# Kernel tuning notes

Hardware: AMD Instinct MI355X
Metric: run time of the kernel (lower is better)

Reference implementation:

```python
import jax, jax.numpy as jnp
import numpy as np

B, A, D, H = 2048, 32, 128, 256

def setup_inputs() -> dict:
    key = jax.random.key(0)
    ks = jax.random.split(key, 12)
    s = lambda fan_in: 1.0 / np.sqrt(fan_in)
    return {
        "obs": jax.random.normal(ks[0], (B, A, D), dtype=jnp.float32),
        "act": jax.random.normal(ks[1], (B, A, 8), dtype=jnp.float32),
        "enc_W": jax.random.uniform(ks[2], (H, D), jnp.float32, -s(D), s(D)),
        "enc_b": jax.random.uniform(ks[3], (H,), jnp.float32, -s(D), s(D)),
        "fobs_W": jax.random.uniform(ks[4], (H, H), jnp.float32, -s(H), s(H)),
        "fobs_b": jax.random.uniform(ks[5], (H,), jnp.float32, -s(H), s(H)),
        "W_ih": jax.random.uniform(ks[6], (3 * H, H), jnp.float32, -s(H), s(H)),
        "b_ih": jax.random.uniform(ks[7], (3 * H,), jnp.float32, -s(H), s(H)),
        "W_hh": jax.random.uniform(ks[8], (3 * H, H), jnp.float32, -s(H), s(H)),
        "b_hh": jax.random.uniform(ks[9], (3 * H,), jnp.float32, -s(H), s(H)),
        "dec_W": jax.random.uniform(ks[10], (1, H), jnp.float32, -s(H), s(H)),
        "dec_b": jax.random.uniform(ks[11], (1,), jnp.float32, -s(H), s(H)),
    }

def _gru_cell(x, h, W_ih, b_ih, W_hh, b_hh):
    # torch.nn.GRUCell: gates stacked as [reset, update, new]
    gi = x @ W_ih.T + b_ih          # [N, 3H]
    gh = h @ W_hh.T + b_hh          # [N, 3H]
    i_r, i_z, i_n = jnp.split(gi, 3, axis=-1)
    h_r, h_z, h_n = jnp.split(gh, 3, axis=-1)
    r = jax.nn.sigmoid(i_r + h_r)
    z = jax.nn.sigmoid(i_z + h_z)
    n = jnp.tanh(i_n + r * h_n)
    return (1.0 - z) * n + z * h

def reference(obs, act, enc_W, enc_b, fobs_W, fobs_b, W_ih, b_ih, W_hh, b_hh, dec_W, dec_b):
    b, a, d = obs.shape
    x = obs.reshape(b * a, d)                         # [B*A, D]
    e = jax.nn.relu(x @ enc_W.T + enc_b)              # encoder + ReLU
    h = e @ fobs_W.T + fobs_b                         # h_out
    # k = 0: comm input is zeros
    h = _gru_cell(jnp.zeros_like(h), h, W_ih, b_ih, W_hh, b_hh)
    # k = 1: masked mean over other agents == (sum_j h_j - h_i) / n_agents
    hA = h.reshape(b, a, -1)                          # [B, A, H]
    c = (hA.sum(axis=1, keepdims=True) - hA) / a      # [B, A, H]
    h = _gru_cell(c.reshape(b * a, -1), h, W_ih, b_ih, W_hh, b_hh)
    return (h @ dec_W.T + dec_b).reshape(b, a, -1)    # [B, A, 1]
```

## Files before the change

kernel.cpp:

```cpp
#include <hip/hip_runtime.h>
#include <hip/hip_fp16.h>


#define NB   2048
#define NA   32
#define DIN  128
#define HID  256
#define SA   264
#define MROWS 64

typedef _Float16 half8  __attribute__((ext_vector_type(8)));
typedef float    float4v __attribute__((ext_vector_type(4)));

#define ENC_OFF    0
#define FOBS_OFF   32768
#define WIH_OFF    98304
#define WHH_OFF    294912
#define PREP_TOTAL 491520

__global__ void prep_weights(const float* __restrict__ encW, const float* __restrict__ fobsW,
                             const float* __restrict__ wih,  const float* __restrict__ whh,
                             _Float16* __restrict__ prep) {
    int G = blockIdx.x * 256 + threadIdx.x;
    if (G >= PREP_TOTAL / 8) return;
    int F = G << 3;
    const float* src; int K, local = F, nt, ks;
    if (F < FOBS_OFF) {
        src = encW;  K = 128;
        int t = local >> 9; nt = t & 15; ks = t >> 4;
    } else if (F < WIH_OFF) {
        src = fobsW; K = 256; local = F - FOBS_OFF;
        int t = local >> 9; nt = t & 15; ks = t >> 4;
    } else if (F < WHH_OFF) {
        src = wih;   K = 256; local = F - WIH_OFF;
        int t = local >> 9; nt = t % 48; ks = t / 48;
    } else {
        src = whh;   K = 256; local = F - WHH_OFF;
        int t = local >> 9; nt = t % 48; ks = t / 48;
    }
    int lane = (local >> 3) & 63;
    int col  = nt * 16 + (lane & 15);
    int k    = ks * 32 + ((lane >> 4) << 3);
    const float* s = src + col * K + k;
    float4v v0 = *(const float4v*)(s);
    float4v v1 = *(const float4v*)(s + 4);
    half8 hv;
    hv[0] = (_Float16)v0[0]; hv[1] = (_Float16)v0[1];
    hv[2] = (_Float16)v0[2]; hv[3] = (_Float16)v0[3];
    hv[4] = (_Float16)v1[0]; hv[5] = (_Float16)v1[1];
    hv[6] = (_Float16)v1[2]; hv[7] = (_Float16)v1[3];
    *(half8*)(prep + F) = hv;
}

__device__ __forceinline__ float sigmoid_f(float x) {
    return 1.f / (1.f + __expf(-x));
}
__device__ __forceinline__ float tanh_f(float x) {
    return 1.f - 2.f / (__expf(2.f * x) + 1.f);
}

__device__ __forceinline__ half8 ldB(const _Float16* __restrict__ prepm, int NT, int nt, int ks,
                                     const float* __restrict__ raw, int K, int use_prep, int lane) {
    if (use_prep)
        return *(const half8*)(prepm + (((ks * NT + nt) * 64 + lane) << 3));
    half8 b;
    int l16 = lane & 15, kq = (lane >> 4) << 3;
    #pragma unroll
    for (int j = 0; j < 8; j++)
        b[j] = (_Float16)raw[(nt * 16 + l16) * K + ks * 32 + kq + j];
    return b;
}

__global__ __launch_bounds__(1024) void commnet_fused(
    const float* __restrict__ obs, const _Float16* __restrict__ prep,
    const float* __restrict__ enc_b, const float* __restrict__ fobs_b,
    const float* __restrict__ b_ih, const float* __restrict__ b_hh,
    const float* __restrict__ dec_W, const float* __restrict__ dec_b,
    float* __restrict__ out,
    const float* __restrict__ encW, const float* __restrict__ fobsW,
    const float* __restrict__ wih, const float* __restrict__ whh,
    int use_prep)
{
    const int b    = blockIdx.x;
    const int tid  = threadIdx.x;
    const int lane = tid & 63;
    const int nt   = tid >> 6;
    const int l16  = lane & 15;
    const int quad = lane >> 4;
    const int kq   = quad << 3;
    const int col  = nt * 16 + l16;

    __shared__ __align__(16) _Float16 sA[3][MROWS * SA];
    __shared__ float Srow[MROWS];

    {
        const float* obsb = obs + (size_t)b * MROWS * DIN;
        int r   = tid >> 4;
        int off = (tid & 15) << 3;
        const float* src = obsb + r * DIN + off;
        float4v v0 = *(const float4v*)(src);
        float4v v1 = *(const float4v*)(src + 4);
        half8 hv;
        hv[0] = (_Float16)v0[0]; hv[1] = (_Float16)v0[1];
        hv[2] = (_Float16)v0[2]; hv[3] = (_Float16)v0[3];
        hv[4] = (_Float16)v1[0]; hv[5] = (_Float16)v1[1];
        hv[6] = (_Float16)v1[2]; hv[7] = (_Float16)v1[3];
        *(half8*)(&sA[0][r * SA + off]) = hv;
        if (tid < MROWS) Srow[tid] = 0.f;
    }
    __syncthreads();

    {
        float4v acc[4];
        float4v z = {0.f, 0.f, 0.f, 0.f};
        acc[0] = z; acc[1] = z; acc[2] = z; acc[3] = z;
        #pragma unroll
        for (int ks = 0; ks < 4; ks++) {
            int kbase = ks * 32 + kq;
            half8 Af[4];
            #pragma unroll
            for (int mt = 0; mt < 4; mt++)
                Af[mt] = *(const half8*)(&sA[0][(mt * 16 + l16) * SA + kbase]);
            half8 b0 = ldB(prep + ENC_OFF, 16, nt, ks, encW, DIN, use_prep, lane);
            #pragma unroll
            for (int mt = 0; mt < 4; mt++)
                acc[mt] = __builtin_amdgcn_mfma_f32_16x16x32_f16(Af[mt], b0, acc[mt], 0, 0, 0);
        }
        float bb = enc_b[col];
        #pragma unroll
        for (int mt = 0; mt < 4; mt++)
            #pragma unroll
            for (int r = 0; r < 4; r++) {
                int row = mt * 16 + quad * 4 + r;
                sA[1][row * SA + col] = (_Float16)fmaxf(acc[mt][r] + bb, 0.f);
            }
    }
    __syncthreads();

    float4v hacc[4];
    {
        float4v z = {0.f, 0.f, 0.f, 0.f};
        hacc[0] = z; hacc[1] = z; hacc[2] = z; hacc[3] = z;
        #pragma unroll 2
        for (int ks = 0; ks < 8; ks++) {
            int kbase = ks * 32 + kq;
            half8 Af[4];
            #pragma unroll
            for (int mt = 0; mt < 4; mt++)
                Af[mt] = *(const half8*)(&sA[1][(mt * 16 + l16) * SA + kbase]);
            half8 b0 = ldB(prep + FOBS_OFF, 16, nt, ks, fobsW, HID, use_prep, lane);
            #pragma unroll
            for (int mt = 0; mt < 4; mt++)
                hacc[mt] = __builtin_amdgcn_mfma_f32_16x16x32_f16(Af[mt], b0, hacc[mt], 0, 0, 0);
        }
        float bb = fobs_b[col];
        #pragma unroll
        for (int mt = 0; mt < 4; mt++)
            #pragma unroll
            for (int r = 0; r < 4; r++) {
                int row = mt * 16 + quad * 4 + r;
                float h = hacc[mt][r] + bb;
                hacc[mt][r] = h;
                sA[0][row * SA + col] = (_Float16)h;
            }
    }
    __syncthreads();

    #pragma unroll 1
    for (int half = 0; half < 2; half++) {
        const int rb = half * 32;
        float4v aR[2], aZ[2], aN[2];
        float4v z = {0.f, 0.f, 0.f, 0.f};
        aR[0] = z; aR[1] = z; aZ[0] = z; aZ[1] = z; aN[0] = z; aN[1] = z;
        #pragma unroll 2
        for (int ks = 0; ks < 8; ks++) {
            const int kbase = ks * 32 + kq;
            half8 A0 = *(const half8*)(&sA[0][(rb + l16) * SA + kbase]);
            half8 A1 = *(const half8*)(&sA[0][(rb + 16 + l16) * SA + kbase]);
            half8 bR = ldB(prep + WHH_OFF, 48,  0 + nt, ks, whh, HID, use_prep, lane);
            half8 bZ = ldB(prep + WHH_OFF, 48, 16 + nt, ks, whh, HID, use_prep, lane);
            half8 bN = ldB(prep + WHH_OFF, 48, 32 + nt, ks, whh, HID, use_prep, lane);
            aR[0] = __builtin_amdgcn_mfma_f32_16x16x32_f16(A0, bR, aR[0], 0, 0, 0);
            aR[1] = __builtin_amdgcn_mfma_f32_16x16x32_f16(A1, bR, aR[1], 0, 0, 0);
            aZ[0] = __builtin_amdgcn_mfma_f32_16x16x32_f16(A0, bZ, aZ[0], 0, 0, 0);
            aZ[1] = __builtin_amdgcn_mfma_f32_16x16x32_f16(A1, bZ, aZ[1], 0, 0, 0);
            aN[0] = __builtin_amdgcn_mfma_f32_16x16x32_f16(A0, bN, aN[0], 0, 0, 0);
            aN[1] = __builtin_amdgcn_mfma_f32_16x16x32_f16(A1, bN, aN[1], 0, 0, 0);
        }
        float biR = b_ih[col],       bhR = b_hh[col];
        float biZ = b_ih[256 + col], bhZ = b_hh[256 + col];
        float biN = b_ih[512 + col], bhN = b_hh[512 + col];
        float h1v[2][4];
        float psum = 0.f;
        #pragma unroll
        for (int mt = 0; mt < 2; mt++)
            #pragma unroll
            for (int r = 0; r < 4; r++) {
                int row = rb + mt * 16 + quad * 4 + r;
                float rg = sigmoid_f(biR + aR[mt][r] + bhR);
                float zg = sigmoid_f(biZ + aZ[mt][r] + bhZ);
                float ng = tanh_f(biN + rg * (aN[mt][r] + bhN));
                float hold = hacc[half * 2 + mt][r];
                float h1 = (1.f - zg) * ng + zg * hold;
                h1v[mt][r] = h1;
                sA[1][row * SA + col] = (_Float16)h1;
                psum += h1;
            }
        psum += __shfl_xor(psum, 16);
        psum += __shfl_xor(psum, 32);
        #pragma unroll
        for (int mt = 0; mt < 2; mt++)
            #pragma unroll
            for (int r = 0; r < 4; r++) {
                int row = rb + mt * 16 + quad * 4 + r;
                sA[2][row * SA + col] = (_Float16)((psum - h1v[mt][r]) * (1.f / 32.f));
            }
    }
    __syncthreads();

    #pragma unroll 1
    for (int half = 0; half < 2; half++) {
        const int rb = half * 32;
        float4v aR[2], aZ[2], aNi[2], aNh[2];
        float4v z = {0.f, 0.f, 0.f, 0.f};
        aR[0] = z; aR[1] = z; aZ[0] = z; aZ[1] = z;
        aNi[0] = z; aNi[1] = z; aNh[0] = z; aNh[1] = z;
        #pragma unroll 1
        for (int ks = 0; ks < 8; ks++) {
            const int kbase = ks * 32 + kq;
            {
                half8 C0 = *(const half8*)(&sA[2][(rb + l16) * SA + kbase]);
                half8 C1 = *(const half8*)(&sA[2][(rb + 16 + l16) * SA + kbase]);
                half8 bR = ldB(prep + WIH_OFF, 48,  0 + nt, ks, wih, HID, use_prep, lane);
                half8 bZ = ldB(prep + WIH_OFF, 48, 16 + nt, ks, wih, HID, use_prep, lane);
                half8 bN = ldB(prep + WIH_OFF, 48, 32 + nt, ks, wih, HID, use_prep, lane);
                aR[0]  = __builtin_amdgcn_mfma_f32_16x16x32_f16(C0, bR, aR[0], 0, 0, 0);
                aR[1]  = __builtin_amdgcn_mfma_f32_16x16x32_f16(C1, bR, aR[1], 0, 0, 0);
                aZ[0]  = __builtin_amdgcn_mfma_f32_16x16x32_f16(C0, bZ, aZ[0], 0, 0, 0);
                aZ[1]  = __builtin_amdgcn_mfma_f32_16x16x32_f16(C1, bZ, aZ[1], 0, 0, 0);
                aNi[0] = __builtin_amdgcn_mfma_f32_16x16x32_f16(C0, bN, aNi[0], 0, 0, 0);
                aNi[1] = __builtin_amdgcn_mfma_f32_16x16x32_f16(C1, bN, aNi[1], 0, 0, 0);
            }
            {
                half8 H0 = *(const half8*)(&sA[1][(rb + l16) * SA + kbase]);
                half8 H1 = *(const half8*)(&sA[1][(rb + 16 + l16) * SA + kbase]);
                half8 bR = ldB(prep + WHH_OFF, 48,  0 + nt, ks, whh, HID, use_prep, lane);
                half8 bZ = ldB(prep + WHH_OFF, 48, 16 + nt, ks, whh, HID, use_prep, lane);
                half8 bN = ldB(prep + WHH_OFF, 48, 32 + nt, ks, whh, HID, use_prep, lane);
                aR[0]  = __builtin_amdgcn_mfma_f32_16x16x32_f16(H0, bR, aR[0], 0, 0, 0);
                aR[1]  = __builtin_amdgcn_mfma_f32_16x16x32_f16(H1, bR, aR[1], 0, 0, 0);
                aZ[0]  = __builtin_amdgcn_mfma_f32_16x16x32_f16(H0, bZ, aZ[0], 0, 0, 0);
                aZ[1]  = __builtin_amdgcn_mfma_f32_16x16x32_f16(H1, bZ, aZ[1], 0, 0, 0);
                aNh[0] = __builtin_amdgcn_mfma_f32_16x16x32_f16(H0, bN, aNh[0], 0, 0, 0);
                aNh[1] = __builtin_amdgcn_mfma_f32_16x16x32_f16(H1, bN, aNh[1], 0, 0, 0);
            }
        }

        float biR = b_ih[col],       bhR = b_hh[col];
        float biZ = b_ih[256 + col], bhZ = b_hh[256 + col];
        float biN = b_ih[512 + col], bhN = b_hh[512 + col];
        float dw  = dec_W[col];
        float p[2][4];
        #pragma unroll
        for (int mt = 0; mt < 2; mt++)
            #pragma unroll
            for (int r = 0; r < 4; r++) {
                int row = rb + mt * 16 + quad * 4 + r;
                float rg = sigmoid_f(aR[mt][r] + biR + bhR);
                float zg = sigmoid_f(aZ[mt][r] + biZ + bhZ);
                float ng = tanh_f((aNi[mt][r] + biN) + rg * (aNh[mt][r] + bhN));
                float h1v = (float)sA[1][row * SA + col];
                float h2 = (1.f - zg) * ng + zg * h1v;
                p[mt][r] = h2 * dw;
            }
        #pragma unroll
        for (int m = 1; m <= 8; m <<= 1) {
            #pragma unroll
            for (int mt = 0; mt < 2; mt++)
                #pragma unroll
                for (int r = 0; r < 4; r++)
                    p[mt][r] += __shfl_xor(p[mt][r], m);
        }
        if (l16 == 0) {
            #pragma unroll
            for (int mt = 0; mt < 2; mt++)
                #pragma unroll
                for (int r = 0; r < 4; r++)
                    atomicAdd(&Srow[rb + mt * 16 + quad * 4 + r], p[mt][r]);
        }
    }
    __syncthreads();
    if (tid < MROWS) out[(size_t)b * MROWS + tid] = Srow[tid] + dec_b[0];
}

extern "C" void kernel_launch(void* const* d_in, const int* in_sizes, int n_in,
                              void* d_out, int out_size, void* d_ws, size_t ws_size,
                              hipStream_t stream) {
    const float* obs   = (const float*)d_in[0];
    const float* encW  = (const float*)d_in[2];
    const float* encb  = (const float*)d_in[3];
    const float* fobsW = (const float*)d_in[4];
    const float* fobsb = (const float*)d_in[5];
    const float* wih   = (const float*)d_in[6];
    const float* bih   = (const float*)d_in[7];
    const float* whh   = (const float*)d_in[8];
    const float* bhh   = (const float*)d_in[9];
    const float* decW  = (const float*)d_in[10];
    const float* decb  = (const float*)d_in[11];
    float* out = (float*)d_out;

    _Float16* prep = (_Float16*)d_ws;
    int use_prep = (ws_size >= (size_t)PREP_TOTAL * sizeof(_Float16)) ? 1 : 0;
    if (use_prep) {
        prep_weights<<<(PREP_TOTAL / 8 + 255) / 256, 256, 0, stream>>>(encW, fobsW, wih, whh, prep);
    }
    commnet_fused<<<NB / 2, 1024, 0, stream>>>(obs, prep, encb, fobsb, bih, bhh, decW, decb, out,
                                               encW, fobsW, wih, whh, use_prep);
}
```

Baseline: 238.2 us.

## Process four batches per block to amortize weight loads across more rows

Each block now handles 128 rows (four batch elements) instead of 64, halving the grid so every weight fragment loaded from global memory feeds twice as many MFMAs. To fit in LDS, the third shared buffer is dropped: the comm input is rebuilt in place from per-group column sums stored in a small float array, and the old hidden state is re-read as fp16 from shared memory rather than kept in fp32 registers. In exchange, fewer blocks cover the device, the reused hidden state loses precision, and extra barriers and passes are added.

```diff
diff --git a/kernel.cpp b/kernel.cpp
--- a/kernel.cpp
+++ b/kernel.cpp
@@ -7,7 +7,7 @@
 #define DIN  128
 #define HID  256
 #define SA   264
-#define MROWS 64
+#define MROWS 128
 
 typedef _Float16 half8  __attribute__((ext_vector_type(8)));
 typedef float    float4v __attribute__((ext_vector_type(4)));
@@ -90,27 +90,34 @@
     const int kq   = quad << 3;
     const int col  = nt * 16 + l16;
 
-    __shared__ __align__(16) _Float16 sA[3][MROWS * SA];
+    __shared__ __align__(16) _Float16 sA[2][MROWS * SA];
+    __shared__ __align__(16) float Scol[4][HID];
     __shared__ float Srow[MROWS];
 
     {
         const float* obsb = obs + (size_t)b * MROWS * DIN;
-        int r   = tid >> 4;
-        int off = (tid & 15) << 3;
-        const float* src = obsb + r * DIN + off;
-        float4v v0 = *(const float4v*)(src);
-        float4v v1 = *(const float4v*)(src + 4);
-        half8 hv;
-        hv[0] = (_Float16)v0[0]; hv[1] = (_Float16)v0[1];
-        hv[2] = (_Float16)v0[2]; hv[3] = (_Float16)v0[3];
-        hv[4] = (_Float16)v1[0]; hv[5] = (_Float16)v1[1];
-        hv[6] = (_Float16)v1[2]; hv[7] = (_Float16)v1[3];
-        *(half8*)(&sA[0][r * SA + off]) = hv;
+        #pragma unroll
+        for (int it = 0; it < 2; it++) {
+            int i   = tid + it * 1024;
+            int r   = i >> 4;
+            int off = (i & 15) << 3;
+            const float* src = obsb + r * DIN + off;
+            float4v v0 = *(const float4v*)(src);
+            float4v v1 = *(const float4v*)(src + 4);
+            half8 hv;
+            hv[0] = (_Float16)v0[0]; hv[1] = (_Float16)v0[1];
+            hv[2] = (_Float16)v0[2]; hv[3] = (_Float16)v0[3];
+            hv[4] = (_Float16)v1[0]; hv[5] = (_Float16)v1[1];
+            hv[6] = (_Float16)v1[2]; hv[7] = (_Float16)v1[3];
+            *(half8*)(&sA[0][r * SA + off]) = hv;
+        }
         if (tid < MROWS) Srow[tid] = 0.f;
     }
     __syncthreads();
 
-    {
+    #pragma unroll 1
+    for (int hp = 0; hp < 2; hp++) {
+        const int rb = hp * 64;
         float4v acc[4];
         float4v z = {0.f, 0.f, 0.f, 0.f};
         acc[0] = z; acc[1] = z; acc[2] = z; acc[3] = z;
@@ -120,7 +127,7 @@
             half8 Af[4];
             #pragma unroll
             for (int mt = 0; mt < 4; mt++)
-                Af[mt] = *(const half8*)(&sA[0][(mt * 16 + l16) * SA + kbase]);
+                Af[mt] = *(const half8*)(&sA[0][(rb + mt * 16 + l16) * SA + kbase]);
             half8 b0 = ldB(prep + ENC_OFF, 16, nt, ks, encW, DIN, use_prep, lane);
             #pragma unroll
             for (int mt = 0; mt < 4; mt++)
@@ -131,44 +138,44 @@
         for (int mt = 0; mt < 4; mt++)
             #pragma unroll
             for (int r = 0; r < 4; r++) {
-                int row = mt * 16 + quad * 4 + r;
+                int row = rb + mt * 16 + quad * 4 + r;
                 sA[1][row * SA + col] = (_Float16)fmaxf(acc[mt][r] + bb, 0.f);
             }
     }
     __syncthreads();
 
-    float4v hacc[4];
-    {
+    #pragma unroll 1
+    for (int hp = 0; hp < 2; hp++) {
+        const int rb = hp * 64;
+        float4v acc[4];
         float4v z = {0.f, 0.f, 0.f, 0.f};
-        hacc[0] = z; hacc[1] = z; hacc[2] = z; hacc[3] = z;
+        acc[0] = z; acc[1] = z; acc[2] = z; acc[3] = z;
         #pragma unroll 2
         for (int ks = 0; ks < 8; ks++) {
             int kbase = ks * 32 + kq;
             half8 Af[4];
             #pragma unroll
             for (int mt = 0; mt < 4; mt++)
-                Af[mt] = *(const half8*)(&sA[1][(mt * 16 + l16) * SA + kbase]);
+                Af[mt] = *(const half8*)(&sA[1][(rb + mt * 16 + l16) * SA + kbase]);
             half8 b0 = ldB(prep + FOBS_OFF, 16, nt, ks, fobsW, HID, use_prep, lane);
             #pragma unroll
             for (int mt = 0; mt < 4; mt++)
-                hacc[mt] = __builtin_amdgcn_mfma_f32_16x16x32_f16(Af[mt], b0, hacc[mt], 0, 0, 0);
+                acc[mt] = __builtin_amdgcn_mfma_f32_16x16x32_f16(Af[mt], b0, acc[mt], 0, 0, 0);
         }
         float bb = fobs_b[col];
         #pragma unroll
         for (int mt = 0; mt < 4; mt++)
             #pragma unroll
             for (int r = 0; r < 4; r++) {
-                int row = mt * 16 + quad * 4 + r;
-                float h = hacc[mt][r] + bb;
-                hacc[mt][r] = h;
-                sA[0][row * SA + col] = (_Float16)h;
+                int row = rb + mt * 16 + quad * 4 + r;
+                sA[0][row * SA + col] = (_Float16)(acc[mt][r] + bb);
             }
     }
     __syncthreads();
 
     #pragma unroll 1
-    for (int half = 0; half < 2; half++) {
-        const int rb = half * 32;
+    for (int q = 0; q < 4; q++) {
+        const int rb = q * 32;
         float4v aR[2], aZ[2], aN[2];
         float4v z = {0.f, 0.f, 0.f, 0.f};
         aR[0] = z; aR[1] = z; aZ[0] = z; aZ[1] = z; aN[0] = z; aN[1] = z;
@@ -190,7 +197,6 @@
         float biR = b_ih[col],       bhR = b_hh[col];
         float biZ = b_ih[256 + col], bhZ = b_hh[256 + col];
         float biN = b_ih[512 + col], bhN = b_hh[512 + col];
-        float h1v[2][4];
         float psum = 0.f;
         #pragma unroll
         for (int mt = 0; mt < 2; mt++)
@@ -200,27 +206,44 @@
                 float rg = sigmoid_f(biR + aR[mt][r] + bhR);
                 float zg = sigmoid_f(biZ + aZ[mt][r] + bhZ);
                 float ng = tanh_f(biN + rg * (aN[mt][r] + bhN));
-                float hold = hacc[half * 2 + mt][r];
+                float hold = (float)sA[0][row * SA + col];
                 float h1 = (1.f - zg) * ng + zg * hold;
-                h1v[mt][r] = h1;
                 sA[1][row * SA + col] = (_Float16)h1;
                 psum += h1;
             }
         psum += __shfl_xor(psum, 16);
         psum += __shfl_xor(psum, 32);
-        #pragma unroll
-        for (int mt = 0; mt < 2; mt++)
-            #pragma unroll
-            for (int r = 0; r < 4; r++) {
-                int row = rb + mt * 16 + quad * 4 + r;
-                sA[2][row * SA + col] = (_Float16)((psum - h1v[mt][r]) * (1.f / 32.f));
-            }
+        if (lane < 16) Scol[q][nt * 16 + lane] = psum;
+    }
+    __syncthreads();
+
+    {
+        #pragma unroll
+        for (int it = 0; it < 4; it++) {
+            int i  = tid + it * 1024;
+            int r  = i >> 5;
+            int c8 = (i & 31) << 3;
+            const float* Sp = &Scol[r >> 5][0];
+            half8 hv = *(const half8*)(&sA[1][r * SA + c8]);
+            float4v t0 = *(const float4v*)(Sp + c8);
+            float4v t1 = *(const float4v*)(Sp + c8 + 4);
+            half8 cv;
+            cv[0] = (_Float16)((t0[0] - (float)hv[0]) * (1.f / 32.f));
+            cv[1] = (_Float16)((t0[1] - (float)hv[1]) * (1.f / 32.f));
+            cv[2] = (_Float16)((t0[2] - (float)hv[2]) * (1.f / 32.f));
+            cv[3] = (_Float16)((t0[3] - (float)hv[3]) * (1.f / 32.f));
+            cv[4] = (_Float16)((t1[0] - (float)hv[4]) * (1.f / 32.f));
+            cv[5] = (_Float16)((t1[1] - (float)hv[5]) * (1.f / 32.f));
+            cv[6] = (_Float16)((t1[2] - (float)hv[6]) * (1.f / 32.f));
+            cv[7] = (_Float16)((t1[3] - (float)hv[7]) * (1.f / 32.f));
+            *(half8*)(&sA[0][r * SA + c8]) = cv;
+        }
     }
     __syncthreads();
 
     #pragma unroll 1
-    for (int half = 0; half < 2; half++) {
-        const int rb = half * 32;
+    for (int q = 0; q < 4; q++) {
+        const int rb = q * 32;
         float4v aR[2], aZ[2], aNi[2], aNh[2];
         float4v z = {0.f, 0.f, 0.f, 0.f};
         aR[0] = z; aR[1] = z; aZ[0] = z; aZ[1] = z;
@@ -229,8 +252,8 @@
         for (int ks = 0; ks < 8; ks++) {
             const int kbase = ks * 32 + kq;
             {
-                half8 C0 = *(const half8*)(&sA[2][(rb + l16) * SA + kbase]);
-                half8 C1 = *(const half8*)(&sA[2][(rb + 16 + l16) * SA + kbase]);
+                half8 C0 = *(const half8*)(&sA[0][(rb + l16) * SA + kbase]);
+                half8 C1 = *(const half8*)(&sA[0][(rb + 16 + l16) * SA + kbase]);
                 half8 bR = ldB(prep + WIH_OFF, 48,  0 + nt, ks, wih, HID, use_prep, lane);
                 half8 bZ = ldB(prep + WIH_OFF, 48, 16 + nt, ks, wih, HID, use_prep, lane);
                 half8 bN = ldB(prep + WIH_OFF, 48, 32 + nt, ks, wih, HID, use_prep, lane);
@@ -314,6 +337,6 @@
     if (use_prep) {
         prep_weights<<<(PREP_TOTAL / 8 + 255) / 256, 256, 0, stream>>>(encW, fobsW, wih, whh, prep);
     }
-    commnet_fused<<<NB / 2, 1024, 0, stream>>>(obs, prep, encb, fobsb, bih, bhh, decW, decb, out,
+    commnet_fused<<<NB / 4, 1024, 0, stream>>>(obs, prep, encb, fobsb, bih, bhh, decW, decb, out,
                                                encW, fobsW, wih, whh, use_prep);
 }
```

Result: slower. 246.2 us (+3.4%).

## Retile fused kernel to one batch per 512-thread block with 2x2 MFMA tiles

Applied to the files above, without the earlier changes.

Each block now handles 32 rows (one batch element) with 8 waves instead of 64 rows with 16 waves, and every wave computes a 2x2 tile of 16x16 MFMA outputs covering two column tiles. This halves LDS per block, so more blocks can be resident per CU and the loop over two row halves disappears, giving more overlap across barriers. Each A fragment is now reused across two weight fragments in registers. The trade-off is that the full weight set is streamed once per 32 rows rather than once per 64 rows, which doubles total weight traffic from L2.

```diff
diff --git a/kernel.cpp b/kernel.cpp
--- a/kernel.cpp
+++ b/kernel.cpp
@@ -7,7 +7,7 @@
 #define DIN  128
 #define HID  256
 #define SA   264
-#define MROWS 64
+#define MROWS 32
 
 typedef _Float16 half8  __attribute__((ext_vector_type(8)));
 typedef float    float4v __attribute__((ext_vector_type(4)));
@@ -71,7 +71,7 @@
     return b;
 }
 
-__global__ __launch_bounds__(1024) void commnet_fused(
+__global__ __launch_bounds__(512) void commnet_fused(
     const float* __restrict__ obs, const _Float16* __restrict__ prep,
     const float* __restrict__ enc_b, const float* __restrict__ fobs_b,
     const float* __restrict__ b_ih, const float* __restrict__ b_hh,
@@ -84,11 +84,11 @@
     const int b    = blockIdx.x;
     const int tid  = threadIdx.x;
     const int lane = tid & 63;
-    const int nt   = tid >> 6;
+    const int w    = tid >> 6;
     const int l16  = lane & 15;
     const int quad = lane >> 4;
     const int kq   = quad << 3;
-    const int col  = nt * 16 + l16;
+    const int nt0  = w * 2;
 
     __shared__ __align__(16) _Float16 sA[3][MROWS * SA];
     __shared__ float Srow[MROWS];
@@ -111,168 +111,219 @@
     __syncthreads();
 
     {
-        float4v acc[4];
+        float4v acc[2][2];
         float4v z = {0.f, 0.f, 0.f, 0.f};
-        acc[0] = z; acc[1] = z; acc[2] = z; acc[3] = z;
+        acc[0][0] = z; acc[0][1] = z; acc[1][0] = z; acc[1][1] = z;
         #pragma unroll
         for (int ks = 0; ks < 4; ks++) {
             int kbase = ks * 32 + kq;
-            half8 Af[4];
-            #pragma unroll
-            for (int mt = 0; mt < 4; mt++)
-                Af[mt] = *(const half8*)(&sA[0][(mt * 16 + l16) * SA + kbase]);
-            half8 b0 = ldB(prep + ENC_OFF, 16, nt, ks, encW, DIN, use_prep, lane);
-            #pragma unroll
-            for (int mt = 0; mt < 4; mt++)
-                acc[mt] = __builtin_amdgcn_mfma_f32_16x16x32_f16(Af[mt], b0, acc[mt], 0, 0, 0);
-        }
-        float bb = enc_b[col];
-        #pragma unroll
-        for (int mt = 0; mt < 4; mt++)
-            #pragma unroll
-            for (int r = 0; r < 4; r++) {
-                int row = mt * 16 + quad * 4 + r;
-                sA[1][row * SA + col] = (_Float16)fmaxf(acc[mt][r] + bb, 0.f);
-            }
-    }
-    __syncthreads();
-
-    float4v hacc[4];
+            half8 A0 = *(const half8*)(&sA[0][(l16) * SA + kbase]);
+            half8 A1 = *(const half8*)(&sA[0][(16 + l16) * SA + kbase]);
+            half8 b0 = ldB(prep + ENC_OFF, 16, nt0,     ks, encW, DIN, use_prep, lane);
+            half8 b1 = ldB(prep + ENC_OFF, 16, nt0 + 1, ks, encW, DIN, use_prep, lane);
+            acc[0][0] = __builtin_amdgcn_mfma_f32_16x16x32_f16(A0, b0, acc[0][0], 0, 0, 0);
+            acc[0][1] = __builtin_amdgcn_mfma_f32_16x16x32_f16(A0, b1, acc[0][1], 0, 0, 0);
+            acc[1][0] = __builtin_amdgcn_mfma_f32_16x16x32_f16(A1, b0, acc[1][0], 0, 0, 0);
+            acc[1][1] = __builtin_amdgcn_mfma_f32_16x16x32_f16(A1, b1, acc[1][1], 0, 0, 0);
+        }
+        #pragma unroll
+        for (int nn = 0; nn < 2; nn++) {
+            int col = (nt0 + nn) * 16 + l16;
+            float bb = enc_b[col];
+            #pragma unroll
+            for (int mt = 0; mt < 2; mt++)
+                #pragma unroll
+                for (int r = 0; r < 4; r++) {
+                    int row = mt * 16 + quad * 4 + r;
+                    sA[1][row * SA + col] = (_Float16)fmaxf(acc[mt][nn][r] + bb, 0.f);
+                }
+        }
+    }
+    __syncthreads();
+
+    float4v hacc[2][2];
     {
         float4v z = {0.f, 0.f, 0.f, 0.f};
-        hacc[0] = z; hacc[1] = z; hacc[2] = z; hacc[3] = z;
+        hacc[0][0] = z; hacc[0][1] = z; hacc[1][0] = z; hacc[1][1] = z;
         #pragma unroll 2
         for (int ks = 0; ks < 8; ks++) {
             int kbase = ks * 32 + kq;
-            half8 Af[4];
-            #pragma unroll
-            for (int mt = 0; mt < 4; mt++)
-                Af[mt] = *(const half8*)(&sA[1][(mt * 16 + l16) * SA + kbase]);
-            half8 b0 = ldB(prep + FOBS_OFF, 16, nt, ks, fobsW, HID, use_prep, lane);
-            #pragma unroll
-            for (int mt = 0; mt < 4; mt++)
-                hacc[mt] = __builtin_amdgcn_mfma_f32_16x16x32_f16(Af[mt], b0, hacc[mt], 0, 0, 0);
-        }
-        float bb = fobs_b[col];
-        #pragma unroll
-        for (int mt = 0; mt < 4; mt++)
-            #pragma unroll
-            for (int r = 0; r < 4; r++) {
-                int row = mt * 16 + quad * 4 + r;
-                float h = hacc[mt][r] + bb;
-                hacc[mt][r] = h;
-                sA[0][row * SA + col] = (_Float16)h;
-            }
-    }
-    __syncthreads();
-
-    #pragma unroll 1
-    for (int half = 0; half < 2; half++) {
-        const int rb = half * 32;
-        float4v aR[2], aZ[2], aN[2];
+            half8 A0 = *(const half8*)(&sA[1][(l16) * SA + kbase]);
+            half8 A1 = *(const half8*)(&sA[1][(16 + l16) * SA + kbase]);
+            half8 b0 = ldB(prep + FOBS_OFF, 16, nt0,     ks, fobsW, HID, use_prep, lane);
+            half8 b1 = ldB(prep + FOBS_OFF, 16, nt0 + 1, ks, fobsW, HID, use_prep, lane);
+            hacc[0][0] = __builtin_amdgcn_mfma_f32_16x16x32_f16(A0, b0, hacc[0][0], 0, 0, 0);
+            hacc[0][1] = __builtin_amdgcn_mfma_f32_16x16x32_f16(A0, b1, hacc[0][1], 0, 0, 0);
+            hacc[1][0] = __builtin_amdgcn_mfma_f32_16x16x32_f16(A1, b0, hacc[1][0], 0, 0, 0);
+            hacc[1][1] = __builtin_amdgcn_mfma_f32_16x16x32_f16(A1, b1, hacc[1][1], 0, 0, 0);
+        }
+        #pragma unroll
+        for (int nn = 0; nn < 2; nn++) {
+            int col = (nt0 + nn) * 16 + l16;
+            float bb = fobs_b[col];
+            #pragma unroll
+            for (int mt = 0; mt < 2; mt++)
+                #pragma unroll
+                for (int r = 0; r < 4; r++) {
+                    int row = mt * 16 + quad * 4 + r;
+                    float h = hacc[mt][nn][r] + bb;
+                    hacc[mt][nn][r] = h;
+                    sA[0][row * SA + col] = (_Float16)h;
+                }
+        }
+    }
+    __syncthreads();
+
+    {
+        float4v aR[2][2], aZ[2][2], aN[2][2];
         float4v z = {0.f, 0.f, 0.f, 0.f};
-        aR[0] = z; aR[1] = z; aZ[0] = z; aZ[1] = z; aN[0] = z; aN[1] = z;
+        #pragma unroll
+        for (int mt = 0; mt < 2; mt++)
+            #pragma unroll
+            for (int nn = 0; nn < 2; nn++) { aR[mt][nn] = z; aZ[mt][nn] = z; aN[mt][nn] = z; }
         #pragma unroll 2
         for (int ks = 0; ks < 8; ks++) {
             const int kbase = ks * 32 + kq;
-            half8 A0 = *(const half8*)(&sA[0][(rb + l16) * SA + kbase]);
-            half8 A1 = *(const half8*)(&sA[0][(rb + 16 + l16) * SA + kbase]);
-            half8 bR = ldB(prep + WHH_OFF, 48,  0 + nt, ks, whh, HID, use_prep, lane);
-            half8 bZ = ldB(prep + WHH_OFF, 48, 16 + nt, ks, whh, HID, use_prep, lane);
-            half8 bN = ldB(prep + WHH_OFF, 48, 32 + nt, ks, whh, HID, use_prep, lane);
-            aR[0] = __builtin_amdgcn_mfma_f32_16x16x32_f16(A0, bR, aR[0], 0, 0, 0);
-            aR[1] = __builtin_amdgcn_mfma_f32_16x16x32_f16(A1, bR, aR[1], 0, 0, 0);
-            aZ[0] = __builtin_amdgcn_mfma_f32_16x16x32_f16(A0, bZ, aZ[0], 0, 0, 0);
-            aZ[1] = __builtin_amdgcn_mfma_f32_16x16x32_f16(A1, bZ, aZ[1], 0, 0, 0);
-            aN[0] = __builtin_amdgcn_mfma_f32_16x16x32_f16(A0, bN, aN[0], 0, 0, 0);
-            aN[1] = __builtin_amdgcn_mfma_f32_16x16x32_f16(A1, bN, aN[1], 0, 0, 0);
-        }
-        float biR = b_ih[col],       bhR = b_hh[col];
-        float biZ = b_ih[256 + col], bhZ = b_hh[256 + col];
-        float biN = b_ih[512 + col], bhN = b_hh[512 + col];
-        float h1v[2][4];
-        float psum = 0.f;
+            half8 A0 = *(const half8*)(&sA[0][(l16) * SA + kbase]);
+            half8 A1 = *(const half8*)(&sA[0][(16 + l16) * SA + kbase]);
+            half8 bR0 = ldB(prep + WHH_OFF, 48,  0 + nt0,     ks, whh, HID, use_prep, lane);
+            half8 bR1 = ldB(prep + WHH_OFF, 48,  0 + nt0 + 1, ks, whh, HID, use_prep, lane);
+            aR[0][0] = __builtin_amdgcn_mfma_f32_16x16x32_f16(A0, bR0, aR[0][0], 0, 0, 0);
+            aR[0][1] = __builtin_amdgcn_mfma_f32_16x16x32_f16(A0, bR1, aR[0][1], 0, 0, 0);
+            aR[1][0] = __builtin_amdgcn_mfma_f32_16x16x32_f16(A1, bR0, aR[1][0], 0, 0, 0);
+            aR[1][1] = __builtin_amdgcn_mfma_f32_16x16x32_f16(A1, bR1, aR[1][1], 0, 0, 0);
+            half8 bZ0 = ldB(prep + WHH_OFF, 48, 16 + nt0,     ks, whh, HID, use_prep, lane);
+            half8 bZ1 = ldB(prep + WHH_OFF, 48, 16 + nt0 + 1, ks, whh, HID, use_prep, lane);
+            aZ[0][0] = __builtin_amdgcn_mfma_f32_16x16x32_f16(A0, bZ0, aZ[0][0], 0, 0, 0);
+            aZ[0][1] = __builtin_amdgcn_mfma_f32_16x16x32_f16(A0, bZ1, aZ[0][1], 0, 0, 0);
+            aZ[1][0] = __builtin_amdgcn_mfma_f32_16x16x32_f16(A1, bZ0, aZ[1][0], 0, 0, 0);
+            aZ[1][1] = __builtin_amdgcn_mfma_f32_16x16x32_f16(A1, bZ1, aZ[1][1], 0, 0, 0);
+            half8 bN0 = ldB(prep + WHH_OFF, 48, 32 + nt0,     ks, whh, HID, use_prep, lane);
+            half8 bN1 = ldB(prep + WHH_OFF, 48, 32 + nt0 + 1, ks, whh, HID, use_prep, lane);
+            aN[0][0] = __builtin_amdgcn_mfma_f32_16x16x32_f16(A0, bN0, aN[0][0], 0, 0, 0);
+            aN[0][1] = __builtin_amdgcn_mfma_f32_16x16x32_f16(A0, bN1, aN[0][1], 0, 0, 0);
+            aN[1][0] = __builtin_amdgcn_mfma_f32_16x16x32_f16(A1, bN0, aN[1][0], 0, 0, 0);
+            aN[1][1] = __builtin_amdgcn_mfma_f32_16x16x32_f16(A1, bN1, aN[1][1], 0, 0, 0);
+        }
+        #pragma unroll
+        for (int nn = 0; nn < 2; nn++) {
+            int col = (nt0 + nn) * 16 + l16;
+            float biR = b_ih[col],       bhR = b_hh[col];
+            float biZ = b_ih[256 + col], bhZ = b_hh[256 + col];
+            float biN = b_ih[512 + col], bhN = b_hh[512 + col];
+            float h1v[2][4];
+            float psum = 0.f;
+            #pragma unroll
+            for (int mt = 0; mt < 2; mt++)
+                #pragma unroll
+                for (int r = 0; r < 4; r++) {
+                    int row = mt * 16 + quad * 4 + r;
+                    float rg = sigmoid_f(biR + aR[mt][nn][r] + bhR);
+                    float zg = sigmoid_f(biZ + aZ[mt][nn][r] + bhZ);
+                    float ng = tanh_f(biN + rg * (aN[mt][nn][r] + bhN));
+                    float hold = hacc[mt][nn][r];
+                    float h1 = (1.f - zg) * ng + zg * hold;
+                    h1v[mt][r] = h1;
+                    sA[1][row * SA + col] = (_Float16)h1;
+                    psum += h1;
+                }
+            psum += __shfl_xor(psum, 16);
+            psum += __shfl_xor(psum, 32);
+            #pragma unroll
+            for (int mt = 0; mt < 2; mt++)
+                #pragma unroll
+                for (int r = 0; r < 4; r++) {
+                    int row = mt * 16 + quad * 4 + r;
+                    sA[2][row * SA + col] = (_Float16)((psum - h1v[mt][r]) * (1.f / 32.f));
+                }
+        }
+    }
+    __syncthreads();
+
+    {
+        float4v aR[2][2], aZ[2][2], aNi[2][2], aNh[2][2];
+        float4v z = {0.f, 0.f, 0.f, 0.f};
         #pragma unroll
         for (int mt = 0; mt < 2; mt++)
             #pragma unroll
-            for (int r = 0; r < 4; r++) {
-                int row = rb + mt * 16 + quad * 4 + r;
-                float rg = sigmoid_f(biR + aR[mt][r] + bhR);
-                float zg = sigmoid_f(biZ + aZ[mt][r] + bhZ);
-                float ng = tanh_f(biN + rg * (aN[mt][r] + bhN));
-                float hold = hacc[half * 2 + mt][r];
-                float h1 = (1.f - zg) * ng + zg * hold;
-                h1v[mt][r] = h1;
-                sA[1][row * SA + col] = (_Float16)h1;
-                psum += h1;
+            for (int nn = 0; nn < 2; nn++) {
+                aR[mt][nn] = z; aZ[mt][nn] = z; aNi[mt][nn] = z; aNh[mt][nn] = z;
             }
-        psum += __shfl_xor(psum, 16);
-        psum += __shfl_xor(psum, 32);
-        #pragma unroll
-        for (int mt = 0; mt < 2; mt++)
-            #pragma unroll
-            for (int r = 0; r < 4; r++) {
-                int row = rb + mt * 16 + quad * 4 + r;
-                sA[2][row * SA + col] = (_Float16)((psum - h1v[mt][r]) * (1.f / 32.f));
-            }
-    }
-    __syncthreads();
-
-    #pragma unroll 1
-    for (int half = 0; half < 2; half++) {
-        const int rb = half * 32;
-        float4v aR[2], aZ[2], aNi[2], aNh[2];
-        float4v z = {0.f, 0.f, 0.f, 0.f};
-        aR[0] = z; aR[1] = z; aZ[0] = z; aZ[1] = z;
-        aNi[0] = z; aNi[1] = z; aNh[0] = z; aNh[1] = z;
         #pragma unroll 1
         for (int ks = 0; ks < 8; ks++) {
             const int kbase = ks * 32 + kq;
             {
-                half8 C0 = *(const half8*)(&sA[2][(rb + l16) * SA + kbase]);
-                half8 C1 = *(const half8*)(&sA[2][(rb + 16 + l16) * SA + kbase]);
-                half8 bR = ldB(prep + WIH_OFF, 48,  0 + nt, ks, wih, HID, use_prep, lane);
-                half8 bZ = ldB(prep + WIH_OFF, 48, 16 + nt, ks, wih, HID, use_prep, lane);
-                half8 bN = ldB(prep + WIH_OFF, 48, 32 + nt, ks, wih, HID, use_prep, lane);
-                aR[0]  = __builtin_amdgcn_mfma_f32_16x16x32_f16(C0, bR, aR[0], 0, 0, 0);
-                aR[1]  = __builtin_amdgcn_mfma_f32_16x16x32_f16(C1, bR, aR[1], 0, 0, 0);
-                aZ[0]  = __builtin_amdgcn_mfma_f32_16x16x32_f16(C0, bZ, aZ[0], 0, 0, 0);
-                aZ[1]  = __builtin_amdgcn_mfma_f32_16x16x32_f16(C1, bZ, aZ[1], 0, 0, 0);
-                aNi[0] = __builtin_amdgcn_mfma_f32_16x16x32_f16(C0, bN, aNi[0], 0, 0, 0);
-                aNi[1] = __builtin_amdgcn_mfma_f32_16x16x32_f16(C1, bN, aNi[1], 0, 0, 0);
+                half8 C0 = *(const half8*)(&sA[2][(l16) * SA + kbase]);
+                half8 C1 = *(const half8*)(&sA[2][(16 + l16) * SA + kbase]);
+                half8 bR0 = ldB(prep + WIH_OFF, 48,  0 + nt0,     ks, wih, HID, use_prep, lane);
+                half8 bR1 = ldB(prep + WIH_OFF, 48,  0 + nt0 + 1, ks, wih, HID, use_prep, lane);
+                aR[0][0]  = __builtin_amdgcn_mfma_f32_16x16x32_f16(C0, bR0, aR[0][0], 0, 0, 0);
+                aR[0][1]  = __builtin_amdgcn_mfma_f32_16x16x32_f16(C0, bR1, aR[0][1], 0, 0, 0);
+                aR[1][0]  = __builtin_amdgcn_mfma_f32_16x16x32_f16(C1, bR0, aR[1][0], 0, 0, 0);
+                aR[1][1]  = __builtin_amdgcn_mfma_f32_16x16x32_f16(C1, bR1, aR[1][1], 0, 0, 0);
+                half8 bZ0 = ldB(prep + WIH_OFF, 48, 16 + nt0,     ks, wih, HID, use_prep, lane);
+                half8 bZ1 = ldB(prep + WIH_OFF, 48, 16 + nt0 + 1, ks, wih, HID, use_prep, lane);
+                aZ[0][0]  = __builtin_amdgcn_mfma_f32_16x16x32_f16(C0, bZ0, aZ[0][0], 0, 0, 0);
+                aZ[0][1]  = __builtin_amdgcn_mfma_f32_16x16x32_f16(C0, bZ1, aZ[0][1], 0, 0, 0);
+                aZ[1][0]  = __builtin_amdgcn_mfma_f32_16x16x32_f16(C1, bZ0, aZ[1][0], 0, 0, 0);
+                aZ[1][1]  = __builtin_amdgcn_mfma_f32_16x16x32_f16(C1, bZ1, aZ[1][1], 0, 0, 0);
+                half8 bN0 = ldB(prep + WIH_OFF, 48, 32 + nt0,     ks, wih, HID, use_prep, lane);
+                half8 bN1 = ldB(prep + WIH_OFF, 48, 32 + nt0 + 1, ks, wih, HID, use_prep, lane);
+                aNi[0][0] = __builtin_amdgcn_mfma_f32_16x16x32_f16(C0, bN0, aNi[0][0], 0, 0, 0);
+                aNi[0][1] = __builtin_amdgcn_mfma_f32_16x16x32_f16(C0, bN1, aNi[0][1], 0, 0, 0);
+                aNi[1][0] = __builtin_amdgcn_mfma_f32_16x16x32_f16(C1, bN0, aNi[1][0], 0, 0, 0);
+                aNi[1][1] = __builtin_amdgcn_mfma_f32_16x16x32_f16(C1, bN1, aNi[1][1], 0, 0, 0);
             }
             {
-                half8 H0 = *(const half8*)(&sA[1][(rb + l16) * SA + kbase]);
-                half8 H1 = *(const half8*)(&sA[1][(rb + 16 + l16) * SA + kbase]);
-                half8 bR = ldB(prep + WHH_OFF, 48,  0 + nt, ks, whh, HID, use_prep, lane);
-                half8 bZ = ldB(prep + WHH_OFF, 48, 16 + nt, ks, whh, HID, use_prep, lane);
-                half8 bN = ldB(prep + WHH_OFF, 48, 32 + nt, ks, whh, HID, use_prep, lane);
-                aR[0]  = __builtin_amdgcn_mfma_f32_16x16x32_f16(H0, bR, aR[0], 0, 0, 0);
-                aR[1]  = __builtin_amdgcn_mfma_f32_16x16x32_f16(H1, bR, aR[1], 0, 0, 0);
-                aZ[0]  = __builtin_amdgcn_mfma_f32_16x16x32_f16(H0, bZ, aZ[0], 0, 0, 0);
-                aZ[1]  = __builtin_amdgcn_mfma_f32_16x16x32_f16(H1, bZ, aZ[1], 0, 0, 0);
-                aNh[0] = __builtin_amdgcn_mfma_f32_16x16x32_f16(H0, bN, aNh[0], 0, 0, 0);
-                aNh[1] = __builtin_amdgcn_mfma_f32_16x16x32_f16(H1, bN, aNh[1], 0, 0, 0);
+                half8 H0 = *(const half8*)(&sA[1][(l16) * SA + kbase]);
+                half8 H1 = *(const half8*)(&sA[1][(16 + l16) * SA + kbase]);
+                half8 bR0 = ldB(prep + WHH_OFF, 48,  0 + nt0,     ks, whh, HID, use_prep, lane);
+                half8 bR1 = ldB(prep + WHH_OFF, 48,  0 + nt0 + 1, ks, whh, HID, use_prep, lane);
+                aR[0][0]  = __builtin_amdgcn_mfma_f32_16x16x32_f16(H0, bR0, aR[0][0], 0, 0, 0);
+                aR[0][1]  = __builtin_amdgcn_mfma_f32_16x16x32_f16(H0, bR1, aR[0][1], 0, 0, 0);
+                aR[1][0]  = __builtin_amdgcn_mfma_f32_16x16x32_f16(H1, bR0, aR[1][0], 0, 0, 0);
+                aR[1][1]  = __builtin_amdgcn_mfma_f32_16x16x32_f16(H1, bR1, aR[1][1], 0, 0, 0);
+                half8 bZ0 = ldB(prep + WHH_OFF, 48, 16 + nt0,     ks, whh, HID, use_prep, lane);
+                half8 bZ1 = ldB(prep + WHH_OFF, 48, 16 + nt0 + 1, ks, whh, HID, use_prep, lane);
+                aZ[0][0]  = __builtin_amdgcn_mfma_f32_16x16x32_f16(H0, bZ0, aZ[0][0], 0, 0, 0);
+                aZ[0][1]  = __builtin_amdgcn_mfma_f32_16x16x32_f16(H0, bZ1, aZ[0][1], 0, 0, 0);
+                aZ[1][0]  = __builtin_amdgcn_mfma_f32_16x16x32_f16(H1, bZ0, aZ[1][0], 0, 0, 0);
+                aZ[1][1]  = __builtin_amdgcn_mfma_f32_16x16x32_f16(H1, bZ1, aZ[1][1], 0, 0, 0);
+                half8 bN0 = ldB(prep + WHH_OFF, 48, 32 + nt0,     ks, whh, HID, use_prep, lane);
+                half8 bN1 = ldB(prep + WHH_OFF, 48, 32 + nt0 + 1, ks, whh, HID, use_prep, lane);
+                aNh[0][0] = __builtin_amdgcn_mfma_f32_16x16x32_f16(H0, bN0, aNh[0][0], 0, 0, 0);
+                aNh[0][1] = __builtin_amdgcn_mfma_f32_16x16x32_f16(H0, bN1, aNh[0][1], 0, 0, 0);
+                aNh[1][0] = __builtin_amdgcn_mfma_f32_16x16x32_f16(H1, bN0, aNh[1][0], 0, 0, 0);
+                aNh[1][1] = __builtin_amdgcn_mfma_f32_16x16x32_f16(H1, bN1, aNh[1][1], 0, 0, 0);
             }
         }
 
-        float biR = b_ih[col],       bhR = b_hh[col];
-        float biZ = b_ih[256 + col], bhZ = b_hh[256 + col];
-        float biN = b_ih[512 + col], bhN = b_hh[512 + col];
-        float dw  = dec_W[col];
         float p[2][4];
         #pragma unroll
         for (int mt = 0; mt < 2; mt++)
             #pragma unroll
-            for (int r = 0; r < 4; r++) {
-                int row = rb + mt * 16 + quad * 4 + r;
-                float rg = sigmoid_f(aR[mt][r] + biR + bhR);
-                float zg = sigmoid_f(aZ[mt][r] + biZ + bhZ);
-                float ng = tanh_f((aNi[mt][r] + biN) + rg * (aNh[mt][r] + bhN));
-                float h1v = (float)sA[1][row * SA + col];
-                float h2 = (1.f - zg) * ng + zg * h1v;
-                p[mt][r] = h2 * dw;
-            }
+            for (int r = 0; r < 4; r++)
+                p[mt][r] = 0.f;
+        #pragma unroll
+        for (int nn = 0; nn < 2; nn++) {
+            int col = (nt0 + nn) * 16 + l16;
+            float biR = b_ih[col],       bhR = b_hh[col];
+            float biZ = b_ih[256 + col], bhZ = b_hh[256 + col];
+            float biN = b_ih[512 + col], bhN = b_hh[512 + col];
+            float dw  = dec_W[col];
+            #pragma unroll
+            for (int mt = 0; mt < 2; mt++)
+                #pragma unroll
+                for (int r = 0; r < 4; r++) {
+                    int row = mt * 16 + quad * 4 + r;
+                    float rg = sigmoid_f(aR[mt][nn][r] + biR + bhR);
+                    float zg = sigmoid_f(aZ[mt][nn][r] + biZ + bhZ);
+                    float ng = tanh_f((aNi[mt][nn][r] + biN) + rg * (aNh[mt][nn][r] + bhN));
+                    float h1v = (float)sA[1][row * SA + col];
+                    float h2 = (1.f - zg) * ng + zg * h1v;
+                    p[mt][r] += h2 * dw;
+                }
+        }
         #pragma unroll
         for (int m = 1; m <= 8; m <<= 1) {
             #pragma unroll
@@ -286,7 +337,7 @@
             for (int mt = 0; mt < 2; mt++)
                 #pragma unroll
                 for (int r = 0; r < 4; r++)
-                    atomicAdd(&Srow[rb + mt * 16 + quad * 4 + r], p[mt][r]);
+                    atomicAdd(&Srow[mt * 16 + quad * 4 + r], p[mt][r]);
         }
     }
     __syncthreads();
@@ -314,6 +365,6 @@
     if (use_prep) {
         prep_weights<<<(PREP_TOTAL / 8 + 255) / 256, 256, 0, stream>>>(encW, fobsW, wih, whh, prep);
     }
-    commnet_fused<<<NB / 2, 1024, 0, stream>>>(obs, prep, encb, fobsb, bih, bhh, decW, decb, out,
-                                               encW, fobsW, wih, whh, use_prep);
-}
+    commnet_fused<<<NB, 512, 0, stream>>>(obs, prep, encb, fobsb, bih, bhh, decW, decb, out,
+                                          encW, fobsW, wih, whh, use_prep);
+}
```

Measured after the change: 292.1 us. 1.23x slower.
